# Kernel optimization log

Measured on AMD Instinct MI355X. Metric: run time of the kernel, lower is better.

## Reference

```python
import jax, jax.numpy as jnp
import numpy as np

NUM_GRAPHS = 64


def setup_inputs() -> dict:
    key = jax.random.key(0)
    ks = jax.random.split(key, 8)
    N, E, D_IN, D_H = 50000, 800000, 128, 256
    x = jax.random.uniform(ks[0], (N, D_IN), dtype=jnp.float32)
    edge_index = jax.random.randint(ks[1], (2, E), 0, N, dtype=jnp.int64)
    batch = jnp.sort(jax.random.randint(ks[2], (N,), 0, NUM_GRAPHS, dtype=jnp.int64))
    s = 1.0 / np.sqrt(D_IN)
    s2 = 1.0 / np.sqrt(D_H)
    W1_rel = jax.random.normal(ks[3], (D_IN, D_H), dtype=jnp.float32) * s
    W1_root = jax.random.normal(ks[4], (D_IN, D_H), dtype=jnp.float32) * s
    b1 = jnp.zeros((D_H,), jnp.float32)
    W2_rel = jax.random.normal(ks[5], (D_H, D_H), dtype=jnp.float32) * s2
    W2_root = jax.random.normal(ks[6], (D_H, D_H), dtype=jnp.float32) * s2
    b2 = jnp.zeros((D_H,), jnp.float32)
    return {"x": x, "edge_index": edge_index, "batch": batch,
            "W1_rel": W1_rel, "W1_root": W1_root, "b1": b1,
            "W2_rel": W2_rel, "W2_root": W2_root, "b2": b2}


def reference(x, edge_index, batch, W1_rel, W1_root, b1, W2_rel, W2_root, b2):
    N = x.shape[0]
    src, dst = edge_index[0], edge_index[1]

    # handcrafted features: per-label fraction of total feature mass + log(graph_size)
    graph_size = jnp.sum(x)
    handcrafted = jnp.concatenate([jnp.sum(x, axis=0) / graph_size,
                                   jnp.log(graph_size)[None]])

    def graph_conv(h, W_rel, W_root, b):
        # PyG GraphConv (aggr='add'): out_i = W_rel @ sum_{j->i} h_j + W_root @ h_i + b
        agg = jax.ops.segment_sum(h[src], dst, num_segments=N)  # [N, d]
        return agg @ W_rel + h @ W_root + b

    h = jax.nn.relu(graph_conv(x, W1_rel, W1_root, b1))
    # layers 2..num_layers share the same weights (module instance reused in original)
    for _ in range(2):
        h = jax.nn.relu(graph_conv(h, W2_rel, W2_root, b2))

    # global_mean_pool over batch ids
    counts = jax.ops.segment_sum(jnp.ones((N,), h.dtype), batch, num_segments=NUM_GRAPHS)
    pooled = jax.ops.segment_sum(h, batch, num_segments=NUM_GRAPHS)
    pooled = pooled / jnp.maximum(counts, 1.0)[:, None]
    return pooled, handcrafted
```

## Files before the change

### kernel.cpp

```cpp
#include <hip/hip_runtime.h>
#include <hip/hip_bf16.h>
#include <string.h>

#define NN 50000
#define NE 800000
#define DIN 128
#define DH 256
#define NG 64
#define PSPLIT 32

typedef short bf16x8 __attribute__((ext_vector_type(8)));
typedef float f32x4 __attribute__((ext_vector_type(4)));

__device__ __forceinline__ float bf2f(__hip_bfloat16 v) { return __bfloat162float(v); }
__device__ __forceinline__ float bfbits(unsigned int lo16) {
  unsigned int u = lo16 << 16;
  float f;
  memcpy(&f, &u, 4);
  return f;
}
__device__ __forceinline__ unsigned int packbf2(float x, float y) {
  __hip_bfloat16 bx = __float2bfloat16(x), by = __float2bfloat16(y);
  unsigned short ux, uy;
  memcpy(&ux, &bx, 2);
  memcpy(&uy, &by, 2);
  return (unsigned int)ux | ((unsigned int)uy << 16);
}

__device__ __forceinline__ float loadF(const void* p, long i, int fbf) {
  return fbf ? bf2f(((const __hip_bfloat16*)p)[i]) : ((const float*)p)[i];
}
__device__ __forceinline__ void storeF(void* p, long i, float v, int fbf) {
  if (fbf) ((__hip_bfloat16*)p)[i] = __float2bfloat16(v);
  else ((float*)p)[i] = v;
}
__device__ __forceinline__ int loadI(const void* p, long i, int i64) {
  return i64 ? (int)((const long long*)p)[i] : ((const int*)p)[i];
}

__global__ void k_detect(const void* x, const void* ei, int* flags) {
  __shared__ int s_f32sig, s_i32sig;
  if (threadIdx.x == 0) { s_f32sig = 0; s_i32sig = 0; }
  __syncthreads();
  int t = threadIdx.x;
  const unsigned short* u = (const unsigned short*)x;
  int f = 0;
  for (int i = 2 * t; i < 8192; i += 512) if (u[i] >= 0x4000) f = 1;
  const unsigned int* w = (const unsigned int*)ei;
  int g = 0;
  for (int i = 2 * t + 1; i < 8192; i += 512) if (w[i] != 0u) g = 1;
  if (f) atomicOr(&s_f32sig, 1);
  if (g) atomicOr(&s_i32sig, 1);
  __syncthreads();
  if (t == 0) { flags[0] = s_f32sig ? 0 : 1; flags[1] = s_i32sig ? 0 : 1; }
}

__global__ void k_zero(int* __restrict__ p, int n) {
  int i = blockIdx.x * blockDim.x + threadIdx.x;
  int stride = gridDim.x * blockDim.x;
  for (; i < n; i += stride) p[i] = 0;
}

__global__ __launch_bounds__(256) void k_prep(
    const void* __restrict__ x, __hip_bfloat16* __restrict__ xb,
    float* __restrict__ colsum, const int* __restrict__ flags) {
  int fbf = flags[0];
  int t = threadIdx.x;
  int lane16 = t & 15;
  int rowoff = t >> 4;
  float acc[8] = {};
  for (int r = blockIdx.x * 16 + rowoff; r < NN; r += gridDim.x * 16) {
    uint4 o;
    if (fbf) {
      uint4 v = ((const uint4*)x)[(long)r * 16 + lane16];
      acc[0] += bfbits(v.x & 0xffffu); acc[1] += bfbits(v.x >> 16);
      acc[2] += bfbits(v.y & 0xffffu); acc[3] += bfbits(v.y >> 16);
      acc[4] += bfbits(v.z & 0xffffu); acc[5] += bfbits(v.z >> 16);
      acc[6] += bfbits(v.w & 0xffffu); acc[7] += bfbits(v.w >> 16);
      o = v;
    } else {
      float4 a = ((const float4*)x)[(long)r * 32 + lane16 * 2];
      float4 b = ((const float4*)x)[(long)r * 32 + lane16 * 2 + 1];
      acc[0] += a.x; acc[1] += a.y; acc[2] += a.z; acc[3] += a.w;
      acc[4] += b.x; acc[5] += b.y; acc[6] += b.z; acc[7] += b.w;
      o.x = packbf2(a.x, a.y); o.y = packbf2(a.z, a.w);
      o.z = packbf2(b.x, b.y); o.w = packbf2(b.z, b.w);
    }
    ((uint4*)xb)[(long)r * 16 + lane16] = o;
  }
  __shared__ float s[16][DIN];
#pragma unroll
  for (int k = 0; k < 8; ++k) s[rowoff][lane16 * 8 + k] = acc[k];
  __syncthreads();
  if (t < DIN) {
    float v = 0.f;
#pragma unroll
    for (int ro = 0; ro < 16; ++ro) v += s[ro][t];
    atomicAdd(&colsum[t], v);
  }
}

__global__ void k_handcrafted(const float* __restrict__ colsum, void* __restrict__ out,
                              const int* __restrict__ flags) {
  __shared__ float s[DIN];
  int fbf = flags[0];
  int t = threadIdx.x;
  s[t] = colsum[t];
  __syncthreads();
  for (int off = DIN / 2; off > 0; off >>= 1) {
    if (t < off) s[t] += s[t + off];
    __syncthreads();
  }
  float g = s[0];
  storeF(out, NG * DH + t, colsum[t] / g, fbf);
  if (t == 0) storeF(out, NG * DH + DIN, logf(g), fbf);
}

__global__ void k_pack_w(const void* __restrict__ Wrel, const void* __restrict__ Wroot,
                         const void* __restrict__ bias, __hip_bfloat16* __restrict__ pack,
                         float* __restrict__ biasf, const int* __restrict__ flags, int K) {
  int fbf = flags[0];
  int KS = K >> 5;
  int total = 2 * K * DH;
  int i = blockIdx.x * blockDim.x + threadIdx.x;
  int stride = gridDim.x * blockDim.x;
  for (int p = i; p < total; p += stride) {
    int m = p / (K * DH);
    int r = p % (K * DH);
    int j = r & 7;
    int l = (r >> 3) & 63;
    int q2 = r >> 9;
    int ks = q2 % KS;
    int ct = q2 / KS;
    int kk = ks * 32 + (l >> 4) * 8 + j;
    int col = ct * 16 + (l & 15);
    const void* W = m ? Wroot : Wrel;
    pack[p] = __float2bfloat16(loadF(W, (long)kk * DH + col, fbf));
  }
  if (i < DH) biasf[i] = loadF(bias, i, fbf);
}

__global__ void k_deg(const void* __restrict__ ei, int* __restrict__ cnt,
                      const int* __restrict__ flags) {
  int i64 = flags[1];
  int e = blockIdx.x * blockDim.x + threadIdx.x;
  int stride = gridDim.x * blockDim.x;
  for (; e < NE; e += stride) {
    int d = loadI(ei, (long)NE + e, i64);
    d = min(max(d, 0), NN - 1);
    atomicAdd(&cnt[d], 1);
  }
}

#define SCAN_B 256
__global__ void k_scan1(const int* __restrict__ cnt, int* __restrict__ rowptr,
                        int* __restrict__ bsum) {
  __shared__ int s[SCAN_B];
  int b = blockIdx.x, t = threadIdx.x;
  int i = b * SCAN_B + t;
  int v = (i < NN) ? cnt[i] : 0;
  s[t] = v;
  __syncthreads();
  for (int off = 1; off < SCAN_B; off <<= 1) {
    int xv = (t >= off) ? s[t - off] : 0;
    __syncthreads();
    s[t] += xv;
    __syncthreads();
  }
  if (i < NN) rowptr[i] = s[t] - v;
  if (t == SCAN_B - 1) bsum[b] = s[t];
}

__global__ void k_scan2(int* __restrict__ bsum, int nb) {
  __shared__ int s[SCAN_B];
  int t = threadIdx.x;
  int v = (t < nb) ? bsum[t] : 0;
  s[t] = v;
  __syncthreads();
  for (int off = 1; off < SCAN_B; off <<= 1) {
    int xv = (t >= off) ? s[t - off] : 0;
    __syncthreads();
    s[t] += xv;
    __syncthreads();
  }
  if (t < nb) bsum[t] = s[t] - v;
}

__global__ void k_scan3(int* __restrict__ rowptr, const int* __restrict__ bsum) {
  int i = blockIdx.x * blockDim.x + threadIdx.x;
  int stride = gridDim.x * blockDim.x;
  for (; i < NN; i += stride) rowptr[i] += bsum[i >> 8];
  if (blockIdx.x == 0 && threadIdx.x == 0) rowptr[NN] = NE;
}

__global__ void k_fill(const void* __restrict__ ei, const int* __restrict__ rowptr,
                       int* __restrict__ cur, int* __restrict__ srcs,
                       const int* __restrict__ flags) {
  int i64 = flags[1];
  int e = blockIdx.x * blockDim.x + threadIdx.x;
  int stride = gridDim.x * blockDim.x;
  for (; e < NE; e += stride) {
    int s = loadI(ei, e, i64);
    int d = loadI(ei, (long)NE + e, i64);
    s = min(max(s, 0), NN - 1);
    d = min(max(d, 0), NN - 1);
    int p = atomicAdd(&cur[d], 1);
    srcs[rowptr[d] + p] = s;
  }
}

__global__ __launch_bounds__(256) void k_gather256(
    const int* __restrict__ rowptr, const int* __restrict__ srcs,
    const __hip_bfloat16* __restrict__ h, __hip_bfloat16* __restrict__ agg) {
  int node = blockIdx.x * 4 + (threadIdx.x >> 6);
  if (node >= NN) return;
  int lane = threadIdx.x & 63;
  int beg = rowptr[node], end = rowptr[node + 1];
  const uint2* h2 = (const uint2*)h;
  float a0 = 0.f, a1 = 0.f, a2 = 0.f, a3 = 0.f;
  int i = beg;
  for (; i + 7 < end; i += 8) {
    uint2 v[8];
#pragma unroll
    for (int u = 0; u < 8; ++u) v[u] = h2[srcs[i + u] * 64 + lane];
#pragma unroll
    for (int u = 0; u < 8; ++u) {
      a0 += bfbits(v[u].x & 0xffffu);
      a1 += bfbits(v[u].x >> 16);
      a2 += bfbits(v[u].y & 0xffffu);
      a3 += bfbits(v[u].y >> 16);
    }
  }
  for (; i < end; ++i) {
    uint2 v0 = h2[srcs[i] * 64 + lane];
    a0 += bfbits(v0.x & 0xffffu);
    a1 += bfbits(v0.x >> 16);
    a2 += bfbits(v0.y & 0xffffu);
    a3 += bfbits(v0.y >> 16);
  }
  uint2 o;
  o.x = packbf2(a0, a1);
  o.y = packbf2(a2, a3);
  ((uint2*)agg)[node * 64 + lane] = o;
}

__global__ __launch_bounds__(256) void k_gather128(
    const int* __restrict__ rowptr, const int* __restrict__ srcs,
    const __hip_bfloat16* __restrict__ h, __hip_bfloat16* __restrict__ agg) {
  int node = blockIdx.x * 4 + (threadIdx.x >> 6);
  if (node >= NN) return;
  int lane = threadIdx.x & 63;
  int beg = rowptr[node], end = rowptr[node + 1];
  const unsigned int* h2 = (const unsigned int*)h;
  float a0 = 0.f, a1 = 0.f;
  int i = beg;
  for (; i + 7 < end; i += 8) {
    unsigned int v[8];
#pragma unroll
    for (int u = 0; u < 8; ++u) v[u] = h2[srcs[i + u] * 64 + lane];
#pragma unroll
    for (int u = 0; u < 8; ++u) {
      a0 += bfbits(v[u] & 0xffffu);
      a1 += bfbits(v[u] >> 16);
    }
  }
  for (; i < end; ++i) {
    unsigned int v0 = h2[srcs[i] * 64 + lane];
    a0 += bfbits(v0 & 0xffffu);
    a1 += bfbits(v0 >> 16);
  }
  ((unsigned int*)agg)[node * 64 + lane] = packbf2(a0, a1);
}

template <int K>
__global__ __launch_bounds__(256, 4) void k_gemm(
    const __hip_bfloat16* __restrict__ A1, const __hip_bfloat16* __restrict__ A2,
    const __hip_bfloat16* __restrict__ Wpack, const float* __restrict__ bias,
    __hip_bfloat16* __restrict__ out) {
  constexpr int KS = K >> 5;
  int lane = threadIdx.x & 63;
  int wave = threadIdx.x >> 6;
  int m15 = lane & 15;
  int q = lane >> 4;
  int row0 = blockIdx.x * 32;
  const short* A1s = (const short*)A1;
  const short* A2s = (const short*)A2;
  const short* Wp = (const short*)Wpack;
  const int wrootOfs = K * DH;
  f32x4 acc[2][4] = {};
#pragma unroll
  for (int ks = 0; ks < KS; ++ks) {
    int kofs = ks * 32 + q * 8;
    bf16x8 a1[2], a2[2], b1[4], b2[4];
#pragma unroll
    for (int mt = 0; mt < 2; ++mt) {
      int r = row0 + mt * 16 + m15;
      if (r > NN - 1) r = NN - 1;
      a1[mt] = *(const bf16x8*)(A1s + r * K + kofs);
      a2[mt] = *(const bf16x8*)(A2s + r * K + kofs);
    }
#pragma unroll
    for (int ct = 0; ct < 4; ++ct) {
      int gct = wave * 4 + ct;
      const short* base = Wp + ((gct * KS + ks) * 64 + lane) * 8;
      b1[ct] = *(const bf16x8*)(base);
      b2[ct] = *(const bf16x8*)(base + wrootOfs);
    }
#pragma unroll
    for (int mt = 0; mt < 2; ++mt)
#pragma unroll
      for (int ct = 0; ct < 4; ++ct) {
        acc[mt][ct] = __builtin_amdgcn_mfma_f32_16x16x32_bf16(a1[mt], b1[ct], acc[mt][ct], 0, 0, 0);
        acc[mt][ct] = __builtin_amdgcn_mfma_f32_16x16x32_bf16(a2[mt], b2[ct], acc[mt][ct], 0, 0, 0);
      }
  }
#pragma unroll
  for (int mt = 0; mt < 2; ++mt)
#pragma unroll
    for (int ct = 0; ct < 4; ++ct) {
      int col = (wave * 4 + ct) * 16 + m15;
      float bv = bias[col];
#pragma unroll
      for (int r = 0; r < 4; ++r) {
        int row = row0 + mt * 16 + q * 4 + r;
        if (row < NN) {
          float v = acc[mt][ct][r] + bv;
          out[row * DH + col] = __float2bfloat16(fmaxf(v, 0.f));
        }
      }
    }
}

__global__ void k_bounds(const void* __restrict__ batch, int* __restrict__ gstart,
                         int* __restrict__ gend, const int* __restrict__ flags) {
  int i64 = flags[1];
  int n = blockIdx.x * blockDim.x + threadIdx.x;
  if (n >= NN) return;
  int b = min(max(loadI(batch, n, i64), 0), NG - 1);
  int bp = (n == 0) ? -1 : min(max(loadI(batch, n - 1, i64), 0), NG - 1);
  if (b != bp) gstart[b] = n;
  int bn = (n == NN - 1) ? -1 : min(max(loadI(batch, n + 1, i64), 0), NG - 1);
  if (b != bn) gend[b] = n + 1;
}

__global__ void k_poolpart(const int* __restrict__ gstart, const int* __restrict__ gend,
                           const __hip_bfloat16* __restrict__ h, float* __restrict__ pooled) {
  int g = blockIdx.x;
  int p = blockIdx.y;
  int j = threadIdx.x;
  int s = gstart[g], e = gend[g];
  int len = e - s;
  if (len <= 0) return;
  int chunk = (len + PSPLIT - 1) / PSPLIT;
  int rs = s + p * chunk;
  int re = min(rs + chunk, e);
  if (rs >= re) return;
  const unsigned int* h2 = (const unsigned int*)h;
  float a0 = 0.f, a1 = 0.f;
  for (int r = rs; r < re; ++r) {
    unsigned int v = h2[(long)r * 128 + j];
    a0 += bfbits(v & 0xffffu);
    a1 += bfbits(v >> 16);
  }
  atomicAdd(&pooled[g * DH + 2 * j], a0);
  atomicAdd(&pooled[g * DH + 2 * j + 1], a1);
}

__global__ void k_poolfin(const int* __restrict__ gstart, const int* __restrict__ gend,
                          const float* __restrict__ pooled, void* __restrict__ out,
                          const int* __restrict__ flags) {
  int fbf = flags[0];
  int g = blockIdx.x;
  int j = threadIdx.x;
  float cnt = fmaxf((float)(gend[g] - gstart[g]), 1.0f);
  storeF(out, (long)g * DH + j, pooled[g * DH + j] / cnt, fbf);
}

extern "C" void kernel_launch(void* const* d_in, const int* in_sizes, int n_in,
                              void* d_out, int out_size, void* d_ws, size_t ws_size,
                              hipStream_t stream) {
  const void* x = d_in[0];
  const void* ei = d_in[1];
  const void* batch = d_in[2];
  const void* W1r = d_in[3];
  const void* W1o = d_in[4];
  const void* b1 = d_in[5];
  const void* W2r = d_in[6];
  const void* W2o = d_in[7];
  const void* b2 = d_in[8];
  void* out = d_out;

  char* w = (char*)d_ws;
  auto alloc = [&](size_t bytes) -> char* {
    char* p = w;
    w += (bytes + 255) & ~(size_t)255;
    return p;
  };
  int* flags = (int*)alloc(64);
  const int zero_n = NN + NN + DIN + NG + NG + NG * DH;
  int* zreg = (int*)alloc((size_t)zero_n * 4);
  int* cnt = zreg;
  int* cur = cnt + NN;
  float* colsum = (float*)(cur + NN);
  int* gstart = (int*)(colsum + DIN);
  int* gend = gstart + NG;
  float* pooled = (float*)(gend + NG);
  int* rowptr = (int*)alloc((NN + 1) * 4);
  int* bsum = (int*)alloc(SCAN_B * 4);
  int* srcs = (int*)alloc((size_t)NE * 4);
  __hip_bfloat16* xb = (__hip_bfloat16*)alloc((size_t)NN * DIN * 2);
  __hip_bfloat16* aggb = (__hip_bfloat16*)alloc((size_t)NN * DH * 2);
  __hip_bfloat16* hA = (__hip_bfloat16*)alloc((size_t)NN * DH * 2);
  __hip_bfloat16* hB = (__hip_bfloat16*)alloc((size_t)NN * DH * 2);
  __hip_bfloat16* wp1 = (__hip_bfloat16*)alloc((size_t)2 * DIN * DH * 2);
  __hip_bfloat16* wp2 = (__hip_bfloat16*)alloc((size_t)2 * DH * DH * 2);
  float* b1f = (float*)alloc(DH * 4);
  float* b2f = (float*)alloc(DH * 4);

  const int nblk = (NN + SCAN_B - 1) / SCAN_B;
  const int gemm_grid = (NN + 31) / 32;
  const int gat_grid = (NN + 3) / 4;

  k_detect<<<1, 256, 0, stream>>>(x, ei, flags);
  k_zero<<<512, 256, 0, stream>>>(zreg, zero_n);

  k_pack_w<<<64, 256, 0, stream>>>(W1r, W1o, b1, wp1, b1f, flags, DIN);
  k_pack_w<<<128, 256, 0, stream>>>(W2r, W2o, b2, wp2, b2f, flags, DH);
  k_prep<<<1024, 256, 0, stream>>>(x, xb, colsum, flags);
  k_handcrafted<<<1, 128, 0, stream>>>(colsum, out, flags);

  k_deg<<<1024, 256, 0, stream>>>(ei, cnt, flags);
  k_scan1<<<nblk, SCAN_B, 0, stream>>>(cnt, rowptr, bsum);
  k_scan2<<<1, SCAN_B, 0, stream>>>(bsum, nblk);
  k_scan3<<<256, 256, 0, stream>>>(rowptr, bsum);
  k_fill<<<1024, 256, 0, stream>>>(ei, rowptr, cur, srcs, flags);

  k_gather128<<<gat_grid, 256, 0, stream>>>(rowptr, srcs, xb, aggb);
  k_gemm<DIN><<<gemm_grid, 256, 0, stream>>>(aggb, xb, wp1, b1f, hA);
  k_gather256<<<gat_grid, 256, 0, stream>>>(rowptr, srcs, hA, aggb);
  k_gemm<DH><<<gemm_grid, 256, 0, stream>>>(aggb, hA, wp2, b2f, hB);
  k_gather256<<<gat_grid, 256, 0, stream>>>(rowptr, srcs, hB, aggb);
  k_gemm<DH><<<gemm_grid, 256, 0, stream>>>(aggb, hB, wp2, b2f, hA);

  k_bounds<<<nblk, 256, 0, stream>>>(batch, gstart, gend, flags);
  k_poolpart<<<dim3(NG, PSPLIT), 128, 0, stream>>>(gstart, gend, hA, pooled);
  k_poolfin<<<NG, DH, 0, stream>>>(gstart, gend, pooled, out, flags);
}
```

Baseline: 496.9 us.

## Fuse neighbor gather into GEMM via shared-memory aggregation tile

Each GraphConv layer's gather and GEMM kernels are merged into one kernel. Each block first sums neighbor features for its 32 rows into a padded LDS tile, then runs the MFMA GEMM reading the aggregate from LDS instead of a global buffer. This removes the global write and read of the aggregate and three kernel launches. The graph-boundary kernel is replaced by binary searches on the sorted batch array inside the pooling kernels. The risks are lower gather parallelism per block and extra LDS use limiting occupancy.

```diff
diff --git a/kernel.cpp b/kernel.cpp
--- a/kernel.cpp
+++ b/kernel.cpp
@@ -36,6 +36,16 @@
 }
 __device__ __forceinline__ int loadI(const void* p, long i, int i64) {
   return i64 ? (int)((const long long*)p)[i] : ((const int*)p)[i];
+}
+
+__device__ __forceinline__ int lb_batch(const void* batch, int i64, int target) {
+  int lo = 0, hi = NN;
+  while (lo < hi) {
+    int mid = (lo + hi) >> 1;
+    if (loadI(batch, mid, i64) < target) lo = mid + 1;
+    else hi = mid;
+  }
+  return lo;
 }
 
 __global__ void k_detect(const void* x, const void* ei, int* flags) {
@@ -209,95 +219,94 @@
   }
 }
 
-__global__ __launch_bounds__(256) void k_gather256(
+template <int K>
+__global__ __launch_bounds__(256, 4) void k_fused(
     const int* __restrict__ rowptr, const int* __restrict__ srcs,
-    const __hip_bfloat16* __restrict__ h, __hip_bfloat16* __restrict__ agg) {
-  int node = blockIdx.x * 4 + (threadIdx.x >> 6);
-  if (node >= NN) return;
-  int lane = threadIdx.x & 63;
-  int beg = rowptr[node], end = rowptr[node + 1];
-  const uint2* h2 = (const uint2*)h;
-  float a0 = 0.f, a1 = 0.f, a2 = 0.f, a3 = 0.f;
-  int i = beg;
-  for (; i + 7 < end; i += 8) {
-    uint2 v[8];
-#pragma unroll
-    for (int u = 0; u < 8; ++u) v[u] = h2[srcs[i + u] * 64 + lane];
-#pragma unroll
-    for (int u = 0; u < 8; ++u) {
-      a0 += bfbits(v[u].x & 0xffffu);
-      a1 += bfbits(v[u].x >> 16);
-      a2 += bfbits(v[u].y & 0xffffu);
-      a3 += bfbits(v[u].y >> 16);
-    }
-  }
-  for (; i < end; ++i) {
-    uint2 v0 = h2[srcs[i] * 64 + lane];
-    a0 += bfbits(v0.x & 0xffffu);
-    a1 += bfbits(v0.x >> 16);
-    a2 += bfbits(v0.y & 0xffffu);
-    a3 += bfbits(v0.y >> 16);
-  }
-  uint2 o;
-  o.x = packbf2(a0, a1);
-  o.y = packbf2(a2, a3);
-  ((uint2*)agg)[node * 64 + lane] = o;
-}
-
-__global__ __launch_bounds__(256) void k_gather128(
-    const int* __restrict__ rowptr, const int* __restrict__ srcs,
-    const __hip_bfloat16* __restrict__ h, __hip_bfloat16* __restrict__ agg) {
-  int node = blockIdx.x * 4 + (threadIdx.x >> 6);
-  if (node >= NN) return;
-  int lane = threadIdx.x & 63;
-  int beg = rowptr[node], end = rowptr[node + 1];
-  const unsigned int* h2 = (const unsigned int*)h;
-  float a0 = 0.f, a1 = 0.f;
-  int i = beg;
-  for (; i + 7 < end; i += 8) {
-    unsigned int v[8];
-#pragma unroll
-    for (int u = 0; u < 8; ++u) v[u] = h2[srcs[i + u] * 64 + lane];
-#pragma unroll
-    for (int u = 0; u < 8; ++u) {
-      a0 += bfbits(v[u] & 0xffffu);
-      a1 += bfbits(v[u] >> 16);
-    }
-  }
-  for (; i < end; ++i) {
-    unsigned int v0 = h2[srcs[i] * 64 + lane];
-    a0 += bfbits(v0 & 0xffffu);
-    a1 += bfbits(v0 >> 16);
-  }
-  ((unsigned int*)agg)[node * 64 + lane] = packbf2(a0, a1);
-}
-
-template <int K>
-__global__ __launch_bounds__(256, 4) void k_gemm(
-    const __hip_bfloat16* __restrict__ A1, const __hip_bfloat16* __restrict__ A2,
+    const __hip_bfloat16* __restrict__ hin,
     const __hip_bfloat16* __restrict__ Wpack, const float* __restrict__ bias,
     __hip_bfloat16* __restrict__ out) {
   constexpr int KS = K >> 5;
+  constexpr int LROW = K + 8;
+  __shared__ short agg[32 * LROW];
   int lane = threadIdx.x & 63;
   int wave = threadIdx.x >> 6;
+  int row0 = blockIdx.x * 32;
+
+  for (int s = 0; s < 8; ++s) {
+    int lr = wave * 8 + s;
+    int node = row0 + lr;
+    float a0 = 0.f, a1 = 0.f, a2 = 0.f, a3 = 0.f;
+    if (node < NN) {
+      int beg = rowptr[node], end = rowptr[node + 1];
+      int i = beg;
+      if constexpr (K == 256) {
+        const uint2* h2 = (const uint2*)hin;
+        for (; i + 7 < end; i += 8) {
+          uint2 v[8];
+#pragma unroll
+          for (int u = 0; u < 8; ++u) v[u] = h2[srcs[i + u] * 64 + lane];
+#pragma unroll
+          for (int u = 0; u < 8; ++u) {
+            a0 += bfbits(v[u].x & 0xffffu);
+            a1 += bfbits(v[u].x >> 16);
+            a2 += bfbits(v[u].y & 0xffffu);
+            a3 += bfbits(v[u].y >> 16);
+          }
+        }
+        for (; i < end; ++i) {
+          uint2 v0 = h2[srcs[i] * 64 + lane];
+          a0 += bfbits(v0.x & 0xffffu);
+          a1 += bfbits(v0.x >> 16);
+          a2 += bfbits(v0.y & 0xffffu);
+          a3 += bfbits(v0.y >> 16);
+        }
+      } else {
+        const unsigned int* h1 = (const unsigned int*)hin;
+        for (; i + 7 < end; i += 8) {
+          unsigned int v[8];
+#pragma unroll
+          for (int u = 0; u < 8; ++u) v[u] = h1[srcs[i + u] * 64 + lane];
+#pragma unroll
+          for (int u = 0; u < 8; ++u) {
+            a0 += bfbits(v[u] & 0xffffu);
+            a1 += bfbits(v[u] >> 16);
+          }
+        }
+        for (; i < end; ++i) {
+          unsigned int v0 = h1[srcs[i] * 64 + lane];
+          a0 += bfbits(v0 & 0xffffu);
+          a1 += bfbits(v0 >> 16);
+        }
+      }
+    }
+    if constexpr (K == 256) {
+      uint2 o;
+      o.x = packbf2(a0, a1);
+      o.y = packbf2(a2, a3);
+      *(uint2*)&agg[lr * LROW + lane * 4] = o;
+    } else {
+      *(unsigned int*)&agg[lr * LROW + lane * 2] = packbf2(a0, a1);
+    }
+  }
+  __syncthreads();
+
   int m15 = lane & 15;
   int q = lane >> 4;
-  int row0 = blockIdx.x * 32;
-  const short* A1s = (const short*)A1;
-  const short* A2s = (const short*)A2;
+  const short* A2s = (const short*)hin;
   const short* Wp = (const short*)Wpack;
   const int wrootOfs = K * DH;
   f32x4 acc[2][4] = {};
 #pragma unroll
   for (int ks = 0; ks < KS; ++ks) {
     int kofs = ks * 32 + q * 8;
-    bf16x8 a1[2], a2[2], b1[4], b2[4];
+    bf16x8 va1[2], va2[2], b1[4], b2[4];
 #pragma unroll
     for (int mt = 0; mt < 2; ++mt) {
-      int r = row0 + mt * 16 + m15;
+      int lr = mt * 16 + m15;
+      va1[mt] = *(const bf16x8*)&agg[lr * LROW + kofs];
+      int r = row0 + lr;
       if (r > NN - 1) r = NN - 1;
-      a1[mt] = *(const bf16x8*)(A1s + r * K + kofs);
-      a2[mt] = *(const bf16x8*)(A2s + r * K + kofs);
+      va2[mt] = *(const bf16x8*)(A2s + r * K + kofs);
     }
 #pragma unroll
     for (int ct = 0; ct < 4; ++ct) {
@@ -310,8 +319,8 @@
     for (int mt = 0; mt < 2; ++mt)
 #pragma unroll
       for (int ct = 0; ct < 4; ++ct) {
-        acc[mt][ct] = __builtin_amdgcn_mfma_f32_16x16x32_bf16(a1[mt], b1[ct], acc[mt][ct], 0, 0, 0);
-        acc[mt][ct] = __builtin_amdgcn_mfma_f32_16x16x32_bf16(a2[mt], b2[ct], acc[mt][ct], 0, 0, 0);
+        acc[mt][ct] = __builtin_amdgcn_mfma_f32_16x16x32_bf16(va1[mt], b1[ct], acc[mt][ct], 0, 0, 0);
+        acc[mt][ct] = __builtin_amdgcn_mfma_f32_16x16x32_bf16(va2[mt], b2[ct], acc[mt][ct], 0, 0, 0);
       }
   }
 #pragma unroll
@@ -331,24 +340,14 @@
     }
 }
 
-__global__ void k_bounds(const void* __restrict__ batch, int* __restrict__ gstart,
-                         int* __restrict__ gend, const int* __restrict__ flags) {
+__global__ void k_poolpart(const void* __restrict__ batch, const __hip_bfloat16* __restrict__ h,
+                           float* __restrict__ pooled, const int* __restrict__ flags) {
   int i64 = flags[1];
-  int n = blockIdx.x * blockDim.x + threadIdx.x;
-  if (n >= NN) return;
-  int b = min(max(loadI(batch, n, i64), 0), NG - 1);
-  int bp = (n == 0) ? -1 : min(max(loadI(batch, n - 1, i64), 0), NG - 1);
-  if (b != bp) gstart[b] = n;
-  int bn = (n == NN - 1) ? -1 : min(max(loadI(batch, n + 1, i64), 0), NG - 1);
-  if (b != bn) gend[b] = n + 1;
-}
-
-__global__ void k_poolpart(const int* __restrict__ gstart, const int* __restrict__ gend,
-                           const __hip_bfloat16* __restrict__ h, float* __restrict__ pooled) {
   int g = blockIdx.x;
   int p = blockIdx.y;
   int j = threadIdx.x;
-  int s = gstart[g], e = gend[g];
+  int s = lb_batch(batch, i64, g);
+  int e = lb_batch(batch, i64, g + 1);
   int len = e - s;
   if (len <= 0) return;
   int chunk = (len + PSPLIT - 1) / PSPLIT;
@@ -366,13 +365,15 @@
   atomicAdd(&pooled[g * DH + 2 * j + 1], a1);
 }
 
-__global__ void k_poolfin(const int* __restrict__ gstart, const int* __restrict__ gend,
-                          const float* __restrict__ pooled, void* __restrict__ out,
-                          const int* __restrict__ flags) {
+__global__ void k_poolfin(const void* __restrict__ batch, const float* __restrict__ pooled,
+                          void* __restrict__ out, const int* __restrict__ flags) {
   int fbf = flags[0];
+  int i64 = flags[1];
   int g = blockIdx.x;
   int j = threadIdx.x;
-  float cnt = fmaxf((float)(gend[g] - gstart[g]), 1.0f);
+  int s = lb_batch(batch, i64, g);
+  int e = lb_batch(batch, i64, g + 1);
+  float cnt = fmaxf((float)(e - s), 1.0f);
   storeF(out, (long)g * DH + j, pooled[g * DH + j] / cnt, fbf);
 }
 
@@ -397,19 +398,16 @@
     return p;
   };
   int* flags = (int*)alloc(64);
-  const int zero_n = NN + NN + DIN + NG + NG + NG * DH;
+  const int zero_n = NN + NN + DIN + NG * DH;
   int* zreg = (int*)alloc((size_t)zero_n * 4);
   int* cnt = zreg;
   int* cur = cnt + NN;
   float* colsum = (float*)(cur + NN);
-  int* gstart = (int*)(colsum + DIN);
-  int* gend = gstart + NG;
-  float* pooled = (float*)(gend + NG);
+  float* pooled = (float*)(colsum + DIN);
   int* rowptr = (int*)alloc((NN + 1) * 4);
   int* bsum = (int*)alloc(SCAN_B * 4);
   int* srcs = (int*)alloc((size_t)NE * 4);
   __hip_bfloat16* xb = (__hip_bfloat16*)alloc((size_t)NN * DIN * 2);
-  __hip_bfloat16* aggb = (__hip_bfloat16*)alloc((size_t)NN * DH * 2);
   __hip_bfloat16* hA = (__hip_bfloat16*)alloc((size_t)NN * DH * 2);
   __hip_bfloat16* hB = (__hip_bfloat16*)alloc((size_t)NN * DH * 2);
   __hip_bfloat16* wp1 = (__hip_bfloat16*)alloc((size_t)2 * DIN * DH * 2);
@@ -418,8 +416,7 @@
   float* b2f = (float*)alloc(DH * 4);
 
   const int nblk = (NN + SCAN_B - 1) / SCAN_B;
-  const int gemm_grid = (NN + 31) / 32;
-  const int gat_grid = (NN + 3) / 4;
+  const int fused_grid = (NN + 31) / 32;
 
   k_detect<<<1, 256, 0, stream>>>(x, ei, flags);
   k_zero<<<512, 256, 0, stream>>>(zreg, zero_n);
@@ -435,14 +432,10 @@
   k_scan3<<<256, 256, 0, stream>>>(rowptr, bsum);
   k_fill<<<1024, 256, 0, stream>>>(ei, rowptr, cur, srcs, flags);
 
-  k_gather128<<<gat_grid, 256, 0, stream>>>(rowptr, srcs, xb, aggb);
-  k_gemm<DIN><<<gemm_grid, 256, 0, stream>>>(aggb, xb, wp1, b1f, hA);
-  k_gather256<<<gat_grid, 256, 0, stream>>>(rowptr, srcs, hA, aggb);
-  k_gemm<DH><<<gemm_grid, 256, 0, stream>>>(aggb, hA, wp2, b2f, hB);
-  k_gather256<<<gat_grid, 256, 0, stream>>>(rowptr, srcs, hB, aggb);
-  k_gemm<DH><<<gemm_grid, 256, 0, stream>>>(aggb, hB, wp2, b2f, hA);
-
-  k_bounds<<<nblk, 256, 0, stream>>>(batch, gstart, gend, flags);
-  k_poolpart<<<dim3(NG, PSPLIT), 128, 0, stream>>>(gstart, gend, hA, pooled);
-  k_poolfin<<<NG, DH, 0, stream>>>(gstart, gend, pooled, out, flags);
-}
+  k_fused<DIN><<<fused_grid, 256, 0, stream>>>(rowptr, srcs, xb, wp1, b1f, hA);
+  k_fused<DH><<<fused_grid, 256, 0, stream>>>(rowptr, srcs, hA, wp2, b2f, hB);
+  k_fused<DH><<<fused_grid, 256, 0, stream>>>(rowptr, srcs, hB, wp2, b2f, hA);
+
+  k_poolpart<<<dim3(NG, PSPLIT), 128, 0, stream>>>(batch, hA, pooled, flags);
+  k_poolfin<<<NG, DH, 0, stream>>>(batch, pooled, out, flags);
+}
```

Result: slower. 539.2 us (+8.5%).
